# Performance work log

Measured on AMD Instinct MI355X. Metric: run time of the kernel, lower is better.

## Reference

```python
import jax, jax.numpy as jnp
import numpy as np

WINDOW_SIZE = 11
SIGMA = 1.5
DATA_RANGE = 1.0
CHANNEL = 3
K1 = 0.01
K2 = 0.03
EPS = 1e-08


def _gaussian_window(window_size, sigma, channel):
    # 1D gaussian normalized to sum 1, then outer product -> 2D window
    xs = np.arange(window_size) - window_size // 2
    g = np.exp(-(xs.astype(np.float32) ** 2) / (2.0 * sigma ** 2))
    g = g / g.sum()
    w2d = np.outer(g, g).astype(np.float32)  # [K, K]
    # depthwise kernel in OIHW layout: [channel, 1, K, K]
    return jnp.asarray(np.broadcast_to(w2d, (channel, 1, window_size, window_size)))


def _depthwise_blur(img, window):
    # img: [B, C, H, W], window: [C, 1, K, K]; SAME padding depthwise conv
    pad = WINDOW_SIZE // 2
    return jax.lax.conv_general_dilated(
        img, window,
        window_strides=(1, 1),
        padding=[(pad, pad), (pad, pad)],
        dimension_numbers=("NCHW", "OIHW", "NCHW"),
        feature_group_count=CHANNEL,
    )


def setup_inputs() -> dict:
    key = jax.random.key(0)
    kx, ky = jax.random.split(key)
    x = jax.random.uniform(kx, (32, 3, 512, 512), dtype=jnp.float32)
    y = jax.random.uniform(ky, (32, 3, 512, 512), dtype=jnp.float32)
    return {"x": x, "y": y}


def reference(x, y):
    window = _gaussian_window(WINDOW_SIZE, SIGMA, CHANNEL)
    C1 = (K1 * DATA_RANGE) ** 2
    C2 = (K2 * DATA_RANGE) ** 2

    mu_x = _depthwise_blur(x, window)
    mu_y = _depthwise_blur(y, window)
    mu_x2 = mu_x * mu_x
    mu_y2 = mu_y * mu_y
    mu_xy = mu_x * mu_y

    sigma_x2 = _depthwise_blur(x * x, window) - mu_x2
    sigma_y2 = _depthwise_blur(y * y, window) - mu_y2
    sigma_xy = _depthwise_blur(x * y, window) - mu_xy

    num = (2.0 * mu_xy + C1) * (2.0 * sigma_xy + C2)
    den = (mu_x2 + mu_y2 + C1) * (sigma_x2 + sigma_y2 + C2)
    ssim_map = num / (den + EPS)
    return 1.0 - jnp.mean(ssim_map)
```

## Files before the change

### kernel.cpp

```cpp
#include <hip/hip_runtime.h>

typedef float v4f   __attribute__((ext_vector_type(4)));
typedef float f32x4 __attribute__((ext_vector_type(4)));
typedef _Float16 h4 __attribute__((ext_vector_type(4)));
typedef _Float16 h8 __attribute__((ext_vector_type(8)));

#define HH 512
#define WW 512
#define NPLANES 96
#define NSTRIP 32
#define NUNIT (NPLANES * NSTRIP)
#define NBLK (NUNIT / 2)
#define C1V 1e-4f
#define C2V 9e-4f
#define EPSV 1e-8f
#define NPIX 25165824.0f

#define SLOT_B 784
#define Q_B    3136
#define WAVE_B 15680
#define LDS_B  31360

#define MF(A, B) __builtin_amdgcn_mfma_f32_16x16x32_f16((A), (B), zf, 0, 0, 0)

#define SELW(DST, IX) { const int ix_ = (IX); float r_ = 0.f; \
  r_ = (ix_ == 0) ? wv0 : r_;  r_ = (ix_ == 1) ? wv1 : r_; \
  r_ = (ix_ == 2) ? wv2 : r_;  r_ = (ix_ == 3) ? wv3 : r_; \
  r_ = (ix_ == 4) ? wv4 : r_;  r_ = (ix_ == 5) ? wv5 : r_; \
  r_ = (ix_ == 6) ? wv6 : r_;  r_ = (ix_ == 7) ? wv7 : r_; \
  r_ = (ix_ == 8) ? wv8 : r_;  r_ = (ix_ == 9) ? wv9 : r_; \
  r_ = (ix_ == 10) ? wv10 : r_; DST = r_; }

#define PACK8(DST, F0,F1,F2,F3,F4,F5,F6,F7) \
  DST = (h8){(_Float16)(F0),(_Float16)(F1),(_Float16)(F2),(_Float16)(F3), \
             (_Float16)(F4),(_Float16)(F5),(_Float16)(F6),(_Float16)(F7)};

#define EPX(M) { \
  const float mux_ = mx[M], muy_ = my[M]; \
  const float mx2_ = mux_ * mux_, my2_ = muy_ * muy_, mxy_ = mux_ * muy_; \
  const float sx2_ = vx2[M] - mx2_, sy2_ = vy2[M] - my2_, sxy_ = vxy[M] - mxy_; \
  const float num_ = fmaf(2.f, mxy_, C1V) * fmaf(2.f, sxy_, C2V); \
  const float den_ = (mx2_ + my2_ + C1V) * (sx2_ + sy2_ + C2V) + EPSV; \
  acc##M = fmaf(num_, __builtin_amdgcn_rcpf(den_), acc##M); }

#define VLOADL(O) { \
  const int c_ = (O) - 1 + ((s + 1) >> 1); \
  const char* rb_ = wlds + (c_ & 3) * SLOT_B + rByte; \
  vbx  = *(const h8*)(rb_); \
  vby  = *(const h8*)(rb_ + Q_B); \
  vbx2 = *(const h8*)(rb_ + 2 * Q_B); \
  vby2 = *(const h8*)(rb_ + 3 * Q_B); \
  vbxy = *(const h8*)(rb_ + 4 * Q_B); }

#define VMFMA { \
  const f32x4 mx  = MF(Wf, vbx);  const f32x4 my  = MF(Wf, vby); \
  const f32x4 vx2 = MF(Wf, vbx2); const f32x4 vy2 = MF(Wf, vby2); \
  const f32x4 vxy = MF(Wf, vbxy); \
  EPX(0) EPX(1) EPX(2) EPX(3) }

#define STEP(TT, CXA,CXB,CYA,CYB) { \
  const int tt_ = (TT); \
  if (tt_ >= 3) VLOADL(tt_ - 3) \
  h8 ax, ay; \
  PACK8(ax, CXA[0],CXA[1],CXA[2],CXA[3], CXB[0],CXB[1],CXB[2],CXB[3]) \
  PACK8(ay, CYA[0],CYA[1],CYA[2],CYA[3], CYB[0],CYB[1],CYB[2],CYB[3]) \
  if (tt_ < 32) { \
    const int rb2_ = min(max(16 * (tt_ + 1), 0), 496); \
    const float* qx_ = xp + (size_t)rb2_ * WW; \
    const float* qy_ = yp + (size_t)rb2_ * WW; \
    CXA = *(const v4f*)(qx_ + offA); CXB = *(const v4f*)(qx_ + offB); \
    CYA = *(const v4f*)(qy_ + offA); CYB = *(const v4f*)(qy_ + offB); \
  } \
  const bool rOK_ = (unsigned)(tt_ - 1) < 32u; \
  const h8 wfh_ = rOK_ ? WfH : (h8)(_Float16)0.f; \
  const h8 ax2 = ax * ax, ay2 = ay * ay, axy = ax * ay; \
  const f32x4 chx  = MF(ax,  wfh_); const f32x4 chy  = MF(ay,  wfh_); \
  const f32x4 chx2 = MF(ax2, wfh_); const f32x4 chy2 = MF(ay2, wfh_); \
  const f32x4 chxy = MF(axy, wfh_); \
  { char* wb_ = wlds + ((tt_ - 1) & 3) * SLOT_B + wByte; \
    *(h4*)(wb_)         = (h4){(_Float16)chx[0], (_Float16)chx[1], (_Float16)chx[2], (_Float16)chx[3]}; \
    *(h4*)(wb_ + Q_B)   = (h4){(_Float16)chy[0], (_Float16)chy[1], (_Float16)chy[2], (_Float16)chy[3]}; \
    *(h4*)(wb_ + 2*Q_B) = (h4){(_Float16)chx2[0],(_Float16)chx2[1],(_Float16)chx2[2],(_Float16)chx2[3]}; \
    *(h4*)(wb_ + 3*Q_B) = (h4){(_Float16)chy2[0],(_Float16)chy2[1],(_Float16)chy2[2],(_Float16)chy2[3]}; \
    *(h4*)(wb_ + 4*Q_B) = (h4){(_Float16)chxy[0],(_Float16)chxy[1],(_Float16)chxy[2],(_Float16)chxy[3]}; } \
  if (tt_ >= 3) VMFMA }

__global__ __launch_bounds__(128)
void ssim_main(const float* __restrict__ x, const float* __restrict__ y,
               float* __restrict__ partial)
{
  __shared__ __attribute__((aligned(16))) char lds[LDS_B];

  const int l = threadIdx.x & 63;
  const int wid = threadIdx.x >> 6;
  const int n = l & 15;
  const int s = l >> 4;

  const int wg = blockIdx.x;
  const int swz = (wg & 7) * (NBLK / 8) + (wg >> 3);
  const int unit = swz * 2 + wid;
  const int plane = unit >> 5;
  const int strip = unit & 31;
  const int C0 = strip * 16;

  char* wlds = lds + wid * WAVE_B;

  const float* xp = x + (size_t)plane * (HH * WW);
  const float* yp = y + (size_t)plane * (HH * WW);

  float wv0, wv1, wv2, wv3, wv4, wv5, wv6, wv7, wv8, wv9, wv10;
#define WINIT(k) wv##k = expf(-((float)((k - 5) * (k - 5))) / 4.5f);
  WINIT(0) WINIT(1) WINIT(2) WINIT(3) WINIT(4) WINIT(5)
  WINIT(6) WINIT(7) WINIT(8) WINIT(9) WINIT(10)
#undef WINIT
  const float inv_ = 1.f / (wv0 + wv1 + wv2 + wv3 + wv4 + wv5 + wv6 + wv7 + wv8 + wv9 + wv10);
#define WNORM(k) wv##k = __int_as_float(__builtin_amdgcn_readfirstlane(__float_as_int(wv##k * inv_)));
  WNORM(0) WNORM(1) WNORM(2) WNORM(3) WNORM(4) WNORM(5)
  WNORM(6) WNORM(7) WNORM(8) WNORM(9) WNORM(10)
#undef WNORM

  const f32x4 zf = {0.f, 0.f, 0.f, 0.f};

  h8 Wf;
  {
    const int kb = 8 * s;
    float b0,b1,b2,b3,b4,b5,b6,b7;
    SELW(b0, kb + 0 - n - 3) SELW(b1, kb + 1 - n - 3)
    SELW(b2, kb + 2 - n - 3) SELW(b3, kb + 3 - n - 3)
    SELW(b4, kb + 4 - n - 3) SELW(b5, kb + 5 - n - 3)
    SELW(b6, kb + 6 - n - 3) SELW(b7, kb + 7 - n - 3)
    PACK8(Wf, b0,b1,b2,b3,b4,b5,b6,b7)
  }

  const int cb = C0 - 8 + 8 * s;
  const bool kill = (cb < 0) || (cb >= WW);
  h8 WfH = Wf;
  if (kill) WfH = (h8)(_Float16)0.f;
  const int ca = kill ? 0 : cb;

  const int offA = n * WW + ca;
  const int offB = offA + 4;

  const int wByte = n * 48 + 8 * s;
  const int rByte = n * 48 + 16 * ((s + 1) & 1);

  h8 vbx, vby, vbx2, vby2, vbxy;
  float acc0 = 0.f, acc1 = 0.f, acc2 = 0.f, acc3 = 0.f;

  v4f XA0, XB0, YA0, YB0, XA1, XB1, YA1, YB1;
  {
    const float* q1x = xp;
    const float* q1y = yp;
    XA0 = *(const v4f*)(q1x + offA); XB0 = *(const v4f*)(q1x + offB);
    YA0 = *(const v4f*)(q1y + offA); YB0 = *(const v4f*)(q1y + offB);
    XA1 = *(const v4f*)(q1x + offA); XB1 = *(const v4f*)(q1x + offB);
    YA1 = *(const v4f*)(q1y + offA); YB1 = *(const v4f*)(q1y + offB);
  }

  #pragma unroll 1
  for (int u = 0; u < 17; ++u) {
    STEP(2 * u,     XA0, XB0, YA0, YB0)
    STEP(2 * u + 1, XA1, XB1, YA1, YB1)
  }
  VLOADL(31) VMFMA

  float a = (acc0 + acc1) + (acc2 + acc3);
  #pragma unroll
  for (int off = 32; off > 0; off >>= 1) a += __shfl_down(a, off);
  if (l == 0) partial[unit] = a;
}

__global__ void finalize_kernel(const float* __restrict__ partial, float* __restrict__ out)
{
  __shared__ float s4[4];
  float a = 0.f;
  for (int i = threadIdx.x; i < NUNIT; i += 256) a += partial[i];
  #pragma unroll
  for (int off = 32; off > 0; off >>= 1) a += __shfl_down(a, off);
  if ((threadIdx.x & 63) == 0) s4[threadIdx.x >> 6] = a;
  __syncthreads();
  if (threadIdx.x == 0) out[0] = 1.f - (s4[0] + s4[1] + s4[2] + s4[3]) * (1.f / NPIX);
}

extern "C" void kernel_launch(void* const* d_in, const int* in_sizes, int n_in,
                              void* d_out, int out_size, void* d_ws, size_t ws_size,
                              hipStream_t stream)
{
  const float* x = (const float*)d_in[0];
  const float* y = (const float*)d_in[1];
  float* ws = (float*)d_ws;
  float* out = (float*)d_out;

  hipLaunchKernelGGL(ssim_main, dim3(NBLK), dim3(128), 0, stream, x, y, ws);
  hipLaunchKernelGGL(finalize_kernel, dim3(1), dim3(256), 0, stream, ws, out);
}
```

Baseline: 68.66 us.

## Stream raw input rows into LDS via async global_load_lds with triple buffering

Replaces register-held prefetch of x/y row tiles with direct global-to-LDS 16-byte async loads into a three-slot ring, gated by s_waitcnt vmcnt. Each workgroup becomes a single wave handling one strip, so LDS per block is one wave's raw plus half-precision buffers. The goal is deeper, register-free prefetch that hides global latency. The cost is extra LDS reads, reliance on vmcnt counting being exact, and smaller workgroups.

```diff
diff --git a/kernel.cpp b/kernel.cpp
--- a/kernel.cpp
+++ b/kernel.cpp
@@ -10,18 +10,25 @@
 #define NPLANES 96
 #define NSTRIP 32
 #define NUNIT (NPLANES * NSTRIP)
-#define NBLK (NUNIT / 2)
 #define C1V 1e-4f
 #define C2V 9e-4f
 #define EPSV 1e-8f
 #define NPIX 25165824.0f
 
-#define SLOT_B 784
-#define Q_B    3136
-#define WAVE_B 15680
-#define LDS_B  31360
+#define RAW_SLOT 5120
+#define RAW_ARR  2560
+#define RAW_ROW  160
+#define HR_BASE  15360
+#define SLOT_B   784
+#define Q_B      3136
+#define LDS_B    31040
 
 #define MF(A, B) __builtin_amdgcn_mfma_f32_16x16x32_f16((A), (B), zf, 0, 0, 0)
+
+__device__ __forceinline__ void gld16(const float* g, char* l) {
+  __builtin_amdgcn_global_load_lds((const __attribute__((address_space(1))) void*)g,
+                                   (__attribute__((address_space(3))) void*)l, 16, 0, 0);
+}
 
 #define SELW(DST, IX) { const int ix_ = (IX); float r_ = 0.f; \
   r_ = (ix_ == 0) ? wv0 : r_;  r_ = (ix_ == 1) ? wv1 : r_; \
@@ -45,7 +52,7 @@
 
 #define VLOADL(O) { \
   const int c_ = (O) - 1 + ((s + 1) >> 1); \
-  const char* rb_ = wlds + (c_ & 3) * SLOT_B + rByte; \
+  const char* rb_ = hlds + (c_ & 3) * SLOT_B + rByte; \
   vbx  = *(const h8*)(rb_); \
   vby  = *(const h8*)(rb_ + Q_B); \
   vbx2 = *(const h8*)(rb_ + 2 * Q_B); \
@@ -58,52 +65,21 @@
   const f32x4 vxy = MF(Wf, vbxy); \
   EPX(0) EPX(1) EPX(2) EPX(3) }
 
-#define STEP(TT, CXA,CXB,CYA,CYB) { \
-  const int tt_ = (TT); \
-  if (tt_ >= 3) VLOADL(tt_ - 3) \
-  h8 ax, ay; \
-  PACK8(ax, CXA[0],CXA[1],CXA[2],CXA[3], CXB[0],CXB[1],CXB[2],CXB[3]) \
-  PACK8(ay, CYA[0],CYA[1],CYA[2],CYA[3], CYB[0],CYB[1],CYB[2],CYB[3]) \
-  if (tt_ < 32) { \
-    const int rb2_ = min(max(16 * (tt_ + 1), 0), 496); \
-    const float* qx_ = xp + (size_t)rb2_ * WW; \
-    const float* qy_ = yp + (size_t)rb2_ * WW; \
-    CXA = *(const v4f*)(qx_ + offA); CXB = *(const v4f*)(qx_ + offB); \
-    CYA = *(const v4f*)(qy_ + offA); CYB = *(const v4f*)(qy_ + offB); \
-  } \
-  const bool rOK_ = (unsigned)(tt_ - 1) < 32u; \
-  const h8 wfh_ = rOK_ ? WfH : (h8)(_Float16)0.f; \
-  const h8 ax2 = ax * ax, ay2 = ay * ay, axy = ax * ay; \
-  const f32x4 chx  = MF(ax,  wfh_); const f32x4 chy  = MF(ay,  wfh_); \
-  const f32x4 chx2 = MF(ax2, wfh_); const f32x4 chy2 = MF(ay2, wfh_); \
-  const f32x4 chxy = MF(axy, wfh_); \
-  { char* wb_ = wlds + ((tt_ - 1) & 3) * SLOT_B + wByte; \
-    *(h4*)(wb_)         = (h4){(_Float16)chx[0], (_Float16)chx[1], (_Float16)chx[2], (_Float16)chx[3]}; \
-    *(h4*)(wb_ + Q_B)   = (h4){(_Float16)chy[0], (_Float16)chy[1], (_Float16)chy[2], (_Float16)chy[3]}; \
-    *(h4*)(wb_ + 2*Q_B) = (h4){(_Float16)chx2[0],(_Float16)chx2[1],(_Float16)chx2[2],(_Float16)chx2[3]}; \
-    *(h4*)(wb_ + 3*Q_B) = (h4){(_Float16)chy2[0],(_Float16)chy2[1],(_Float16)chy2[2],(_Float16)chy2[3]}; \
-    *(h4*)(wb_ + 4*Q_B) = (h4){(_Float16)chxy[0],(_Float16)chxy[1],(_Float16)chxy[2],(_Float16)chxy[3]}; } \
-  if (tt_ >= 3) VMFMA }
-
-__global__ __launch_bounds__(128)
+__global__ __launch_bounds__(64)
 void ssim_main(const float* __restrict__ x, const float* __restrict__ y,
                float* __restrict__ partial)
 {
   __shared__ __attribute__((aligned(16))) char lds[LDS_B];
 
-  const int l = threadIdx.x & 63;
-  const int wid = threadIdx.x >> 6;
+  const int l = threadIdx.x;
   const int n = l & 15;
   const int s = l >> 4;
 
   const int wg = blockIdx.x;
-  const int swz = (wg & 7) * (NBLK / 8) + (wg >> 3);
-  const int unit = swz * 2 + wid;
-  const int plane = unit >> 5;
-  const int strip = unit & 31;
+  const int swz = (wg & 7) * (NUNIT / 8) + (wg >> 3);
+  const int plane = swz >> 5;
+  const int strip = swz & 31;
   const int C0 = strip * 16;
-
-  char* wlds = lds + wid * WAVE_B;
 
   const float* xp = x + (size_t)plane * (HH * WW);
   const float* yp = y + (size_t)plane * (HH * WW);
@@ -136,38 +112,81 @@
   const bool kill = (cb < 0) || (cb >= WW);
   h8 WfH = Wf;
   if (kill) WfH = (h8)(_Float16)0.f;
-  const int ca = kill ? 0 : cb;
-
-  const int offA = n * WW + ca;
-  const int offB = offA + 4;
+
+  const float *pQ0, *pQ1, *pQ2, *pQ3, *pQ4;
+#define MKQ(Q, P) { \
+  const int o_ = (Q) * 1024 + 16 * l; \
+  const int a_ = o_ / RAW_ARR; \
+  const int rem_ = o_ % RAW_ARR; \
+  const int r_ = rem_ / RAW_ROW; \
+  const int cf_ = (rem_ % RAW_ROW) >> 2; \
+  const int ca_ = min(max(C0 - 8 + cf_, 0), WW - 4); \
+  P = (a_ ? yp : xp) + r_ * WW + ca_; }
+  MKQ(0, pQ0) MKQ(1, pQ1) MKQ(2, pQ2) MKQ(3, pQ3) MKQ(4, pQ4)
+#undef MKQ
 
   const int wByte = n * 48 + 8 * s;
   const int rByte = n * 48 + 16 * ((s + 1) & 1);
+  const int rawOff = n * RAW_ROW + 32 * s;
+  char* hlds = lds + HR_BASE;
 
   h8 vbx, vby, vbx2, vby2, vbxy;
   float acc0 = 0.f, acc1 = 0.f, acc2 = 0.f, acc3 = 0.f;
 
-  v4f XA0, XB0, YA0, YB0, XA1, XB1, YA1, YB1;
-  {
-    const float* q1x = xp;
-    const float* q1y = yp;
-    XA0 = *(const v4f*)(q1x + offA); XB0 = *(const v4f*)(q1x + offB);
-    YA0 = *(const v4f*)(q1y + offA); YB0 = *(const v4f*)(q1y + offB);
-    XA1 = *(const v4f*)(q1x + offA); XB1 = *(const v4f*)(q1x + offB);
-    YA1 = *(const v4f*)(q1y + offA); YB1 = *(const v4f*)(q1y + offB);
+  #pragma unroll
+  for (int k = 0; k < 3; ++k) {
+    char* db = lds + k * RAW_SLOT;
+    const int off = k * 8192;
+    gld16(pQ0 + off, db);        gld16(pQ1 + off, db + 1024);
+    gld16(pQ2 + off, db + 2048); gld16(pQ3 + off, db + 3072);
+    gld16(pQ4 + off, db + 4096);
   }
 
   #pragma unroll 1
-  for (int u = 0; u < 17; ++u) {
-    STEP(2 * u,     XA0, XB0, YA0, YB0)
-    STEP(2 * u + 1, XA1, XB1, YA1, YB1)
+  for (int tt = 0; tt < 34; ++tt) {
+    if (tt >= 3) { VLOADL(tt - 3) }
+
+    { const int d = min(tt + 1, 31);
+      char* db = lds + (d % 3) * RAW_SLOT;
+      const int off = d * 8192;
+      gld16(pQ0 + off, db);        gld16(pQ1 + off, db + 1024);
+      gld16(pQ2 + off, db + 2048); gld16(pQ3 + off, db + 3072);
+      gld16(pQ4 + off, db + 4096); }
+    asm volatile("s_waitcnt vmcnt(10)" ::: "memory");
+
+    const int c = min(max(tt - 1, 0), 31);
+    const char* rb = lds + (c % 3) * RAW_SLOT + rawOff;
+    const v4f xr0 = *(const v4f*)(rb);
+    const v4f xr1 = *(const v4f*)(rb + 16);
+    const v4f yr0 = *(const v4f*)(rb + RAW_ARR);
+    const v4f yr1 = *(const v4f*)(rb + RAW_ARR + 16);
+
+    h8 ax, ay;
+    PACK8(ax, xr0[0],xr0[1],xr0[2],xr0[3], xr1[0],xr1[1],xr1[2],xr1[3])
+    PACK8(ay, yr0[0],yr0[1],yr0[2],yr0[3], yr1[0],yr1[1],yr1[2],yr1[3])
+    const bool rOK = (unsigned)(tt - 1) < 32u;
+    const h8 wfh = rOK ? WfH : (h8)(_Float16)0.f;
+    const h8 ax2 = ax * ax, ay2 = ay * ay, axy = ax * ay;
+    const f32x4 chx  = MF(ax,  wfh); const f32x4 chy  = MF(ay,  wfh);
+    const f32x4 chx2 = MF(ax2, wfh); const f32x4 chy2 = MF(ay2, wfh);
+    const f32x4 chxy = MF(axy, wfh);
+    { char* wb = hlds + ((tt - 1) & 3) * SLOT_B + wByte;
+      *(h4*)(wb)         = (h4){(_Float16)chx[0], (_Float16)chx[1], (_Float16)chx[2], (_Float16)chx[3]};
+      *(h4*)(wb + Q_B)   = (h4){(_Float16)chy[0], (_Float16)chy[1], (_Float16)chy[2], (_Float16)chy[3]};
+      *(h4*)(wb + 2*Q_B) = (h4){(_Float16)chx2[0],(_Float16)chx2[1],(_Float16)chx2[2],(_Float16)chx2[3]};
+      *(h4*)(wb + 3*Q_B) = (h4){(_Float16)chy2[0],(_Float16)chy2[1],(_Float16)chy2[2],(_Float16)chy2[3]};
+      *(h4*)(wb + 4*Q_B) = (h4){(_Float16)chxy[0],(_Float16)chxy[1],(_Float16)chxy[2],(_Float16)chxy[3]}; }
+
+    if (tt >= 3) { VMFMA }
   }
   VLOADL(31) VMFMA
+
+  asm volatile("s_waitcnt vmcnt(0)" ::: "memory");
 
   float a = (acc0 + acc1) + (acc2 + acc3);
   #pragma unroll
   for (int off = 32; off > 0; off >>= 1) a += __shfl_down(a, off);
-  if (l == 0) partial[unit] = a;
+  if (l == 0) partial[swz] = a;
 }
 
 __global__ void finalize_kernel(const float* __restrict__ partial, float* __restrict__ out)
@@ -191,6 +210,6 @@
   float* ws = (float*)d_ws;
   float* out = (float*)d_out;
 
-  hipLaunchKernelGGL(ssim_main, dim3(NBLK), dim3(128), 0, stream, x, y, ws);
+  hipLaunchKernelGGL(ssim_main, dim3(NUNIT), dim3(64), 0, stream, x, y, ws);
   hipLaunchKernelGGL(finalize_kernel, dim3(1), dim3(256), 0, stream, ws, out);
 }
```

New measurement: 73.22 us. 6.6% more time.
